# Performance work log

Measured on AMD Instinct MI355X. Metric: run time of the kernel, lower is better.

Reference implementation:

```python
import jax, jax.numpy as jnp
import numpy as np

B, T, C = 2, 2048, 2048
N_HEAD, N_KV_HEAD = 16, 4
HEAD_DIM = C // N_HEAD  # 128
EPS = 1e-6


def rms_norm(x):
    # no learned scale, normalize over head_dim (last axis)
    return x * jax.lax.rsqrt(jnp.mean(jnp.square(x), axis=-1, keepdims=True) + EPS)


def apply_rotary_emb(x, cos, sin):
    # x: [B, T, H, D]; cos/sin: [T, D/2]  (rotate-half RoPE)
    x1, x2 = jnp.split(x, 2, axis=-1)
    c = cos[None, :, None, :]
    s = sin[None, :, None, :]
    return jnp.concatenate([x1 * c - x2 * s, x1 * s + x2 * c], axis=-1)


def setup_inputs() -> dict:
    key = jax.random.key(0)
    ks = jax.random.split(key, 6)
    x = jax.random.normal(ks[0], (B, T, C), dtype=jnp.float32)
    # real rotary tables: theta = 10000^{-2i/D}
    inv_freq = 1.0 / (10000.0 ** (jnp.arange(0, HEAD_DIM, 2, dtype=jnp.float32) / HEAD_DIM))
    angles = jnp.arange(T, dtype=jnp.float32)[:, None] * inv_freq[None, :]  # [T, D/2]
    cos, sin = jnp.cos(angles), jnp.sin(angles)
    std = 0.02
    Wq = jax.random.normal(ks[1], (C, N_HEAD * HEAD_DIM), dtype=jnp.float32) * std
    Wk = jax.random.normal(ks[2], (C, N_KV_HEAD * HEAD_DIM), dtype=jnp.float32) * std
    Wv = jax.random.normal(ks[3], (C, N_KV_HEAD * HEAD_DIM), dtype=jnp.float32) * std
    Wp = jax.random.normal(ks[4], (C, C), dtype=jnp.float32) * std
    return {"x": x, "cos": cos, "sin": sin, "Wq": Wq, "Wk": Wk, "Wv": Wv, "Wp": Wp}


def reference(x, cos, sin, Wq, Wk, Wv, Wp):
    Bx, Tx, Cx = x.shape
    q = (x @ Wq).reshape(Bx, Tx, N_HEAD, HEAD_DIM)
    k = (x @ Wk).reshape(Bx, Tx, N_KV_HEAD, HEAD_DIM)
    v = (x @ Wv).reshape(Bx, Tx, N_KV_HEAD, HEAD_DIM)
    q = rms_norm(apply_rotary_emb(q, cos, sin))
    k = rms_norm(apply_rotary_emb(k, cos, sin))
    # module scales q by 1/sqrt(D) AND nn.dot_product_attention scales again
    q = q * (1.0 / jnp.sqrt(HEAD_DIM))
    # GQA head repeat
    n_rep = N_HEAD // N_KV_HEAD
    k = jnp.repeat(k, n_rep, axis=2)  # [B, T, H, D]
    v = jnp.repeat(v, n_rep, axis=2)
    scores = jnp.einsum("bthd,bshd->bhts", q, k) / jnp.sqrt(jnp.asarray(HEAD_DIM, x.dtype))
    causal = jnp.tril(jnp.ones((Tx, Tx), dtype=bool))  # key <= query
    scores = jnp.where(causal[None, None, :, :], scores, jnp.finfo(scores.dtype).min)
    probs = jax.nn.softmax(scores, axis=-1)
    y = jnp.einsum("bhts,bshd->bthd", probs, v).reshape(Bx, Tx, Cx)
    return y @ Wp
```

## Files before the change

### kernel.cpp

```cpp
#include <hip/hip_runtime.h>
#include <hip/hip_bf16.h>
#include <math.h>

#define B_  2
#define T_  2048
#define C_  2048
#define NH_ 16
#define NKV_ 4
#define HD_ 128
#define NREP_ (NH_/NKV_)

#define QKVLD 3072
#define KOFF  2048
#define VOFF  2560

#define QSCALE 0.01127105500694502f

typedef __bf16 bf16x8 __attribute__((ext_vector_type(8)));
typedef float  f32x4  __attribute__((ext_vector_type(4)));

__device__ inline void gload_lds16(const void* g, void* l) {
    __builtin_amdgcn_global_load_lds((const __attribute__((address_space(1))) void*)g,
                                     (__attribute__((address_space(3))) void*)l, 16, 0, 0);
}

__global__ __launch_bounds__(256) void cast_bf16(const float* __restrict__ src,
                                                 __bf16* __restrict__ dst)
{
    size_t i = ((size_t)blockIdx.x * 256 + threadIdx.x) * 8;
    float4 a = *(const float4*)&src[i];
    float4 b = *(const float4*)&src[i + 4];
    union { __bf16 h[8]; uint4 u; } pk;
    pk.h[0] = (__bf16)a.x; pk.h[1] = (__bf16)a.y; pk.h[2] = (__bf16)a.z; pk.h[3] = (__bf16)a.w;
    pk.h[4] = (__bf16)b.x; pk.h[5] = (__bf16)b.y; pk.h[6] = (__bf16)b.z; pk.h[7] = (__bf16)b.w;
    *(uint4*)&dst[i] = pk.u;
}

__global__ __launch_bounds__(256) void wtrans_qkv(const float* __restrict__ Wq,
                                                  const float* __restrict__ Wk,
                                                  const float* __restrict__ Wv,
                                                  __bf16* __restrict__ dst)
{
    __shared__ float tl[32][33];
    int ct = blockIdx.x;
    int k0 = blockIdx.y * 32;
    const float* src;
    int ncols, c0, dr0;
    if (ct < 64)      { src = Wq; ncols = 2048; c0 = ct * 32;        dr0 = ct * 32; }
    else if (ct < 80) { src = Wk; ncols = 512;  c0 = (ct - 64) * 32; dr0 = KOFF + (ct - 64) * 32; }
    else              { src = Wv; ncols = 512;  c0 = (ct - 80) * 32; dr0 = VOFF + (ct - 80) * 32; }

    int tid = threadIdx.x;
    int r  = tid >> 3;
    int c4 = (tid & 7) * 4;
    float4 v = *(const float4*)&src[(size_t)(k0 + r) * ncols + c0 + c4];
    tl[r][c4] = v.x; tl[r][c4 + 1] = v.y; tl[r][c4 + 2] = v.z; tl[r][c4 + 3] = v.w;
    __syncthreads();
    union { __bf16 h[4]; uint2 u; } pk;
#pragma unroll
    for (int j = 0; j < 4; ++j) pk.h[j] = (__bf16)tl[c4 + j][r];
    *(uint2*)&dst[(size_t)(dr0 + r) * 2048 + k0 + c4] = pk.u;
}

__global__ __launch_bounds__(256) void wtrans(const float* __restrict__ src,
                                              __bf16* __restrict__ dst, int ncols)
{
    __shared__ float tl[32][33];
    int n0 = blockIdx.x * 32;
    int k0 = blockIdx.y * 32;
    int tid = threadIdx.x;
    int r  = tid >> 3;
    int c4 = (tid & 7) * 4;
    float4 v = *(const float4*)&src[(size_t)(k0 + r) * ncols + n0 + c4];
    tl[r][c4] = v.x; tl[r][c4 + 1] = v.y; tl[r][c4 + 2] = v.z; tl[r][c4 + 3] = v.w;
    __syncthreads();
    union { __bf16 h[4]; uint2 u; } pk;
#pragma unroll
    for (int j = 0; j < 4; ++j) pk.h[j] = (__bf16)tl[c4 + j][r];
    *(uint2*)&dst[(size_t)(n0 + r) * 2048 + k0 + c4] = pk.u;
}

template<typename TOUT>
__global__ __launch_bounds__(256) void gemm_bt(const __bf16* __restrict__ A,
                                               const __bf16* __restrict__ Bt,
                                               TOUT* __restrict__ C,
                                               int M, int N, int K, int ldc)
{
    __shared__ __bf16 As[2][128 * 32];
    __shared__ __bf16 Bs[2][128 * 32];

    const int tid  = threadIdx.x;
    const int wv   = tid >> 6;
    const int lane = tid & 63;
    const int grp  = lane >> 4;
    const int id16 = lane & 15;
    const int wr   = wv >> 1;
    const int wc   = wv & 1;

    const int row0 = blockIdx.y * 128;
    const int col0 = blockIdx.x * 128;

    const int sm = tid >> 2;
    const int sk = (tid & 3) << 3;

    const __bf16* ga0 = A  + (size_t)(row0 + sm) * K + sk;
    const __bf16* ga1 = A  + (size_t)(row0 + 64 + sm) * K + sk;
    const __bf16* gb0 = Bt + (size_t)(col0 + sm) * K + sk;
    const __bf16* gb1 = Bt + (size_t)(col0 + 64 + sm) * K + sk;

    f32x4 acc[4][4];
    const f32x4 fz = {0.f, 0.f, 0.f, 0.f};
#pragma unroll
    for (int i = 0; i < 4; ++i)
#pragma unroll
        for (int j = 0; j < 4; ++j) acc[i][j] = fz;

    const int nk = K >> 5;

    {
        __bf16* a0 = &As[0][wv << 9];
        __bf16* b0 = &Bs[0][wv << 9];
        gload_lds16(ga0, a0);
        gload_lds16(ga1, a0 + 2048);
        gload_lds16(gb0, b0);
        gload_lds16(gb1, b0 + 2048);
    }

    for (int kt = 0; kt < nk; ++kt) {
        const int bufc = kt & 1;
        asm volatile("s_waitcnt vmcnt(0)" ::: "memory");
        __syncthreads();

        if (kt + 1 < nk) {
            const int kb = (kt + 1) << 5;
            __bf16* a0 = &As[1 - bufc][wv << 9];
            __bf16* b0 = &Bs[1 - bufc][wv << 9];
            gload_lds16(ga0 + kb, a0);
            gload_lds16(ga1 + kb, a0 + 2048);
            gload_lds16(gb0 + kb, b0);
            gload_lds16(gb1 + kb, b0 + 2048);
        }

        bf16x8 af[4], bfr[4];
#pragma unroll
        for (int i = 0; i < 4; ++i)
            af[i] = *(const bf16x8*)&As[bufc][((wr << 6) + (i << 4) + id16) * 32 + (grp << 3)];
#pragma unroll
        for (int j = 0; j < 4; ++j)
            bfr[j] = *(const bf16x8*)&Bs[bufc][((wc << 6) + (j << 4) + id16) * 32 + (grp << 3)];
#pragma unroll
        for (int i = 0; i < 4; ++i)
#pragma unroll
            for (int j = 0; j < 4; ++j)
                acc[i][j] = __builtin_amdgcn_mfma_f32_16x16x32_bf16(af[i], bfr[j], acc[i][j], 0, 0, 0);
    }

#pragma unroll
    for (int i = 0; i < 4; ++i) {
        int gr = row0 + (wr << 6) + (i << 4) + (grp << 2);
#pragma unroll
        for (int j = 0; j < 4; ++j) {
            int gc = col0 + (wc << 6) + (j << 4) + id16;
#pragma unroll
            for (int r = 0; r < 4; ++r) {
                if constexpr (sizeof(TOUT) == 4)
                    C[(size_t)(gr + r) * ldc + gc] = acc[i][j][r];
                else
                    C[(size_t)(gr + r) * ldc + gc] = (TOUT)acc[i][j][r];
            }
        }
    }
}

__global__ __launch_bounds__(256) void rope_rms_b(__bf16* __restrict__ base,
                                                  const float* __restrict__ cosb,
                                                  const float* __restrict__ sinb,
                                                  int nheads, float scale)
{
    int wid  = blockIdx.x * 4 + (threadIdx.x >> 6);
    int lane = threadIdx.x & 63;
    int bt = wid / nheads;
    int hd = wid % nheads;
    int t  = bt % T_;

    __bf16* p = base + (size_t)bt * QKVLD + hd * HD_;
    float c = cosb[t * 64 + lane];
    float s = sinb[t * 64 + lane];
    float x1 = (float)p[lane];
    float x2 = (float)p[lane + 64];
    float r1 = x1 * c - x2 * s;
    float r2 = x1 * s + x2 * c;
    float ss = r1 * r1 + r2 * r2;
#pragma unroll
    for (int off = 32; off; off >>= 1) ss += __shfl_xor(ss, off, 64);
    float inv = rsqrtf(ss * (1.f / 128.f) + 1e-6f) * scale;
    p[lane]      = (__bf16)(r1 * inv);
    p[lane + 64] = (__bf16)(r2 * inv);
}

__global__ __launch_bounds__(256) void vtrans(const __bf16* __restrict__ qkv,
                                              __bf16* __restrict__ vt)
{
    __shared__ __bf16 tl[32][HD_ + 8];
    int bx  = blockIdx.x;
    int st  = bx & 63;
    int bkv = bx >> 6;
    int b = bkv >> 2, kv = bkv & 3;
    int s0 = st << 5;
    int tid = threadIdx.x;
    {
        int s = tid >> 3;
        int d = (tid & 7) << 4;
        const __bf16* src = qkv + (size_t)(b * T_ + s0 + s) * QKVLD + VOFF + kv * HD_ + d;
        *(bf16x8*)&tl[s][d]     = *(const bf16x8*)src;
        *(bf16x8*)&tl[s][d + 8] = *(const bf16x8*)(src + 8);
    }
    __syncthreads();
    {
        int d  = tid >> 1;
        int sh = (tid & 1) << 4;
        __bf16 tmp[16];
#pragma unroll
        for (int j = 0; j < 16; ++j) tmp[j] = tl[sh + j][d];
        __bf16* dst = vt + ((size_t)(b * NKV_ + kv) * HD_ + d) * T_ + s0 + sh;
        *(bf16x8*)dst       = *(bf16x8*)&tmp[0];
        *(bf16x8*)(dst + 8) = *(bf16x8*)&tmp[8];
    }
}

#define KT2 64
#define PP  72

__global__ __launch_bounds__(256) void attn_mfma2(const __bf16* __restrict__ qkv,
                                                  const __bf16* __restrict__ vbT,
                                                  __bf16* __restrict__ y)
{
    __shared__ __bf16 Ks[2][KT2 * 128];
    __shared__ __bf16 VTs[2][128 * KT2];
    __shared__ __bf16 Ps[4][16 * PP];

    const int tid  = threadIdx.x;
    const int wv   = tid >> 6;
    const int lane = tid & 63;
    const int grp  = lane >> 4;
    const int id16 = lane & 15;

    const int bx = blockIdx.x;
    const int j  = bx & 15;
    const int bh = bx >> 4;
    const int b  = bh >> 4;
    const int h  = bh & 15;
    const int kv = h >> 2;

    const int q0a = j << 6;
    const int q0b = (31 - j) << 6;
    const int NTa = j + 1;
    const int NT  = 33;

    const int l4 = lane >> 4, l8 = lane >> 3;
    size_t koff[4], voff[4];
#pragma unroll
    for (int i = 0; i < 4; ++i) {
        int key = wv * 16 + i * 4 + l4;
        int ch  = (lane & 15) ^ (i * 4 + l4);
        koff[i] = (size_t)key * (QKVLD * 2) + ch * 16;
        int d   = wv * 32 + i * 8 + l8;
        int ch2 = (lane & 7) ^ l8;
        voff[i] = (size_t)d * (T_ * 2) + ch2 * 16;
    }
    const char* kg = (const char*)(qkv + (size_t)b * T_ * QKVLD + KOFF + kv * HD_);
    const char* vg = (const char*)(vbT + ((size_t)(b * NKV_ + kv) * HD_) * T_);

    bf16x8 qf[4], qf2[4];
    {
        const __bf16* qp = qkv + (size_t)(b * T_ + q0a + wv * 16 + id16) * QKVLD + h * HD_ + (grp << 3);
#pragma unroll
        for (int c = 0; c < 4; ++c) qf[c] = *(const bf16x8*)(qp + c * 32);
        const __bf16* qp2 = qkv + (size_t)(b * T_ + q0b + wv * 16 + id16) * QKVLD + h * HD_ + (grp << 3);
#pragma unroll
        for (int c = 0; c < 4; ++c) qf2[c] = *(const bf16x8*)(qp2 + c * 32);
    }

    const f32x4 fz = {0.f, 0.f, 0.f, 0.f};
    f32x4 o[8];
#pragma unroll
    for (int c = 0; c < 8; ++c) o[c] = fz;
    float l_r[4];
#pragma unroll
    for (int r = 0; r < 4; ++r) l_r[r] = 0.f;

    int qbase = q0a + wv * 16;
    int q0c   = q0a;

    {
        __bf16* kl = &Ks[0][(wv * 16) * 128];
        __bf16* vl = &VTs[0][(wv * 32) * 64];
#pragma unroll
        for (int i = 0; i < 4; ++i) gload_lds16(kg + koff[i], kl + i * 4 * 128);
#pragma unroll
        for (int i = 0; i < 4; ++i) gload_lds16(vg + voff[i], vl + i * 8 * 64);
    }

    for (int tt = 0; tt < NT; ++tt) {
        const int bufc = tt & 1;
        asm volatile("s_waitcnt vmcnt(0)" ::: "memory");
        __syncthreads();

        if (tt + 1 < NT) {
            int tn = tt + 1;
            int sn = (tn >= NTa ? tn - NTa : tn) << 6;
            __bf16* kl = &Ks[tn & 1][(wv * 16) * 128];
            __bf16* vl = &VTs[tn & 1][(wv * 32) * 64];
            const char* kp = kg + (size_t)sn * (QKVLD * 2);
            const char* vp = vg + (size_t)sn * 2;
#pragma unroll
            for (int i = 0; i < 4; ++i) gload_lds16(kp + koff[i], kl + i * 4 * 128);
#pragma unroll
            for (int i = 0; i < 4; ++i) gload_lds16(vp + voff[i], vl + i * 8 * 64);
        }

        if (tt == NTa) {
            float inv[4];
#pragma unroll
            for (int r = 0; r < 4; ++r) {
                float l = l_r[r];
                l += __shfl_xor(l, 1, 64);
                l += __shfl_xor(l, 2, 64);
                l += __shfl_xor(l, 4, 64);
                l += __shfl_xor(l, 8, 64);
                inv[r] = 1.f / l;
            }
#pragma unroll
            for (int r = 0; r < 4; ++r) {
                int q = qbase + (grp << 2) + r;
                __bf16* yp = y + (size_t)(b * T_ + q) * C_ + h * HD_ + id16;
#pragma unroll
                for (int c = 0; c < 8; ++c) yp[c * 16] = (__bf16)(o[c][r] * inv[r]);
            }
#pragma unroll
            for (int c = 0; c < 8; ++c) o[c] = fz;
#pragma unroll
            for (int r = 0; r < 4; ++r) l_r[r] = 0.f;
#pragma unroll
            for (int c = 0; c < 4; ++c) qf[c] = qf2[c];
            qbase = q0b + wv * 16;
            q0c   = q0b;
        }

        const int s0 = (tt >= NTa ? tt - NTa : tt) << 6;

        f32x4 S[4];
#pragma unroll
        for (int t = 0; t < 4; ++t) S[t] = fz;
#pragma unroll
        for (int c = 0; c < 4; ++c) {
#pragma unroll
            for (int t = 0; t < 4; ++t) {
                bf16x8 kf = *(const bf16x8*)&Ks[bufc][(t * 16 + id16) * 128 + ((((c << 2) + grp) ^ id16) << 3)];
                S[t] = __builtin_amdgcn_mfma_f32_16x16x32_bf16(qf[c], kf, S[t], 0, 0, 0);
            }
        }
        if (s0 == q0c) {
#pragma unroll
            for (int t = 0; t < 4; ++t)
#pragma unroll
                for (int r = 0; r < 4; ++r)
                    if (s0 + t * 16 + id16 > qbase + (grp << 2) + r) S[t][r] = -1e30f;
        }

#pragma unroll
        for (int t = 0; t < 4; ++t)
#pragma unroll
            for (int r = 0; r < 4; ++r) S[t][r] = exp2f(S[t][r]);
#pragma unroll
        for (int r = 0; r < 4; ++r)
            l_r[r] += (S[0][r] + S[1][r]) + (S[2][r] + S[3][r]);

        __bf16* pw = Ps[wv];
#pragma unroll
        for (int t = 0; t < 4; ++t)
#pragma unroll
            for (int r = 0; r < 4; ++r)
                pw[((grp << 2) + r) * PP + t * 16 + id16] = (__bf16)S[t][r];

        asm volatile("s_waitcnt lgkmcnt(0)" ::: "memory");
        bf16x8 pf0 = *(const bf16x8*)&pw[id16 * PP + (grp << 3)];
        bf16x8 pf1 = *(const bf16x8*)&pw[id16 * PP + 32 + (grp << 3)];

#pragma unroll
        for (int c2 = 0; c2 < 8; ++c2) {
            bf16x8 vf0 = *(const bf16x8*)&VTs[bufc][(c2 * 16 + id16) * 64 + ((grp ^ (id16 & 7)) << 3)];
            o[c2] = __builtin_amdgcn_mfma_f32_16x16x32_bf16(pf0, vf0, o[c2], 0, 0, 0);
            bf16x8 vf1 = *(const bf16x8*)&VTs[bufc][(c2 * 16 + id16) * 64 + (((4 + grp) ^ (id16 & 7)) << 3)];
            o[c2] = __builtin_amdgcn_mfma_f32_16x16x32_bf16(pf1, vf1, o[c2], 0, 0, 0);
        }
    }

    {
        float inv[4];
#pragma unroll
        for (int r = 0; r < 4; ++r) {
            float l = l_r[r];
            l += __shfl_xor(l, 1, 64);
            l += __shfl_xor(l, 2, 64);
            l += __shfl_xor(l, 4, 64);
            l += __shfl_xor(l, 8, 64);
            inv[r] = 1.f / l;
        }
#pragma unroll
        for (int r = 0; r < 4; ++r) {
            int q = qbase + (grp << 2) + r;
            __bf16* yp = y + (size_t)(b * T_ + q) * C_ + h * HD_ + id16;
#pragma unroll
            for (int c = 0; c < 8; ++c) yp[c * 16] = (__bf16)(o[c][r] * inv[r]);
        }
    }
}

extern "C" void kernel_launch(void* const* d_in, const int* in_sizes, int n_in,
                              void* d_out, int out_size, void* d_ws, size_t ws_size,
                              hipStream_t stream)
{
    const float* x    = (const float*)d_in[0];
    const float* cosb = (const float*)d_in[1];
    const float* sinb = (const float*)d_in[2];
    const float* Wq   = (const float*)d_in[3];
    const float* Wk   = (const float*)d_in[4];
    const float* Wv   = (const float*)d_in[5];
    const float* Wp   = (const float*)d_in[6];
    float* out = (float*)d_out;

    const int M = B_ * T_;

    char* w = (char*)d_ws;
    __bf16* xb    = (__bf16*)w;  w += (size_t)M * C_ * 2;
    __bf16* qkv   = (__bf16*)w;  w += (size_t)M * QKVLD * 2;
    __bf16* wqkvT = (__bf16*)w;  w += (size_t)QKVLD * C_ * 2;
    __bf16* wpT   = (__bf16*)w;  w += (size_t)C_ * C_ * 2;
    __bf16* vt    = (__bf16*)w;  w += (size_t)M * NKV_ * HD_ * 2;
    __bf16* y     = (__bf16*)w;

    cast_bf16<<<(M * C_) / 2048, 256, 0, stream>>>(x, xb);
    wtrans_qkv<<<dim3(96, C_ / 32), 256, 0, stream>>>(Wq, Wk, Wv, wqkvT);
    wtrans<<<dim3(C_ / 32, C_ / 32), 256, 0, stream>>>(Wp, wpT, C_);

    gemm_bt<__bf16><<<dim3(QKVLD / 128, M / 128), 256, 0, stream>>>(xb, wqkvT, qkv, M, QKVLD, C_, QKVLD);

    rope_rms_b<<<(M * NH_) / 4, 256, 0, stream>>>(qkv, cosb, sinb, NH_, QSCALE);
    rope_rms_b<<<(M * NKV_) / 4, 256, 0, stream>>>(qkv + KOFF, cosb, sinb, NKV_, 1.0f);

    vtrans<<<B_ * NKV_ * (T_ / 32), 256, 0, stream>>>(qkv, vt);

    attn_mfma2<<<B_ * NH_ * 16, 256, 0, stream>>>(qkv, vt, y);

    gemm_bt<float><<<dim3(C_ / 128, M / 128), 256, 0, stream>>>(y, wpT, out, M, C_, C_, C_);
}
```

Measured before the change: 318.9 us.

## Rewrite attention with 32x32 MFMA, register-resident P, and 128-row query blocks

Replaces the 16x16 MFMA attention kernel with one that uses 32x32x16 MFMA tiles. Each block now handles 128 query rows, with 32 per wave, and blocks are ordered heaviest first in place of the paired light/heavy query scheme. The kernel computes S transposed (K as the A operand) so probabilities can be repacked in registers via a cross-half lane shuffle, removing the LDS round-trip for P. It also adds setprio around the MFMA bursts and a launch bound of two blocks per CU. The cost is more registers, some waves idling on fully masked tiles (they skip with continue), and a different load balance.

```diff
diff --git a/kernel.cpp b/kernel.cpp
--- a/kernel.cpp
+++ b/kernel.cpp
@@ -18,6 +18,7 @@
 
 typedef __bf16 bf16x8 __attribute__((ext_vector_type(8)));
 typedef float  f32x4  __attribute__((ext_vector_type(4)));
+typedef float  f32x16 __attribute__((ext_vector_type(16)));
 
 __device__ inline void gload_lds16(const void* g, void* l) {
     __builtin_amdgcn_global_load_lds((const __attribute__((address_space(1))) void*)g,
@@ -228,77 +229,65 @@
     }
 }
 
-#define KT2 64
-#define PP  72
-
-__global__ __launch_bounds__(256) void attn_mfma2(const __bf16* __restrict__ qkv,
-                                                  const __bf16* __restrict__ vbT,
-                                                  __bf16* __restrict__ y)
-{
-    __shared__ __bf16 Ks[2][KT2 * 128];
-    __shared__ __bf16 VTs[2][128 * KT2];
-    __shared__ __bf16 Ps[4][16 * PP];
+__global__ __launch_bounds__(256, 2) void attn32(const __bf16* __restrict__ qkv,
+                                                 const __bf16* __restrict__ vbT,
+                                                 __bf16* __restrict__ y)
+{
+    __shared__ __bf16 Ks[2][64 * 128];
+    __shared__ __bf16 Vs[2][64 * 128];
 
     const int tid  = threadIdx.x;
     const int wv   = tid >> 6;
     const int lane = tid & 63;
-    const int grp  = lane >> 4;
-    const int id16 = lane & 15;
-
-    const int bx = blockIdx.x;
-    const int j  = bx & 15;
-    const int bh = bx >> 4;
-    const int b  = bh >> 4;
-    const int h  = bh & 15;
-    const int kv = h >> 2;
-
-    const int q0a = j << 6;
-    const int q0b = (31 - j) << 6;
-    const int NTa = j + 1;
-    const int NT  = 33;
-
-    const int l4 = lane >> 4, l8 = lane >> 3;
+    const int l31  = lane & 31;
+    const int h32  = lane >> 5;
+
+    const int bx    = blockIdx.x;
+    const int jslot = bx >> 5;
+    const int bh    = bx & 31;
+    const int b     = bh >> 4;
+    const int h     = bh & 15;
+    const int kv    = h >> 2;
+    const int jj    = (jslot < 8) ? (15 - jslot) : (jslot - 8);
+
+    const int NT  = 2 * jj + 2;
+    const int qw0 = jj * 128 + wv * 32;
+    const int qme = qw0 + l31;
+
     size_t koff[4], voff[4];
 #pragma unroll
     for (int i = 0; i < 4; ++i) {
-        int key = wv * 16 + i * 4 + l4;
-        int ch  = (lane & 15) ^ (i * 4 + l4);
-        koff[i] = (size_t)key * (QKVLD * 2) + ch * 16;
-        int d   = wv * 32 + i * 8 + l8;
-        int ch2 = (lane & 7) ^ l8;
-        voff[i] = (size_t)d * (T_ * 2) + ch2 * 16;
+        int r  = (wv * 4 + i) * 4 + (lane >> 4);
+        int c  = lane & 15;
+        int cs = c ^ (r & 15);
+        koff[i] = (size_t)r * (QKVLD * 2) + (size_t)cs * 16;
+        int d   = r + ((cs >> 3) << 6);
+        voff[i] = (size_t)d * (T_ * 2) + (size_t)(cs & 7) * 16;
     }
     const char* kg = (const char*)(qkv + (size_t)b * T_ * QKVLD + KOFF + kv * HD_);
     const char* vg = (const char*)(vbT + ((size_t)(b * NKV_ + kv) * HD_) * T_);
 
-    bf16x8 qf[4], qf2[4];
+    bf16x8 qf[8];
     {
-        const __bf16* qp = qkv + (size_t)(b * T_ + q0a + wv * 16 + id16) * QKVLD + h * HD_ + (grp << 3);
-#pragma unroll
-        for (int c = 0; c < 4; ++c) qf[c] = *(const bf16x8*)(qp + c * 32);
-        const __bf16* qp2 = qkv + (size_t)(b * T_ + q0b + wv * 16 + id16) * QKVLD + h * HD_ + (grp << 3);
-#pragma unroll
-        for (int c = 0; c < 4; ++c) qf2[c] = *(const bf16x8*)(qp2 + c * 32);
-    }
-
-    const f32x4 fz = {0.f, 0.f, 0.f, 0.f};
-    f32x4 o[8];
-#pragma unroll
-    for (int c = 0; c < 8; ++c) o[c] = fz;
-    float l_r[4];
-#pragma unroll
-    for (int r = 0; r < 4; ++r) l_r[r] = 0.f;
-
-    int qbase = q0a + wv * 16;
-    int q0c   = q0a;
+        const __bf16* qp = qkv + (size_t)(b * T_ + qw0 + l31) * QKVLD + h * HD_ + h32 * 8;
+#pragma unroll
+        for (int s = 0; s < 8; ++s) qf[s] = *(const bf16x8*)(qp + s * 16);
+    }
+
+    f32x16 o[4];
+#pragma unroll
+    for (int dt = 0; dt < 4; ++dt)
+#pragma unroll
+        for (int r = 0; r < 16; ++r) o[dt][r] = 0.f;
+    float l_p = 0.f;
 
     {
-        __bf16* kl = &Ks[0][(wv * 16) * 128];
-        __bf16* vl = &VTs[0][(wv * 32) * 64];
-#pragma unroll
-        for (int i = 0; i < 4; ++i) gload_lds16(kg + koff[i], kl + i * 4 * 128);
-#pragma unroll
-        for (int i = 0; i < 4; ++i) gload_lds16(vg + voff[i], vl + i * 8 * 64);
+        __bf16* kl = &Ks[0][(wv * 4) * 512];
+        __bf16* vl = &Vs[0][(wv * 4) * 512];
+#pragma unroll
+        for (int i = 0; i < 4; ++i) gload_lds16(kg + koff[i], kl + i * 512);
+#pragma unroll
+        for (int i = 0; i < 4; ++i) gload_lds16(vg + voff[i], vl + i * 512);
     }
 
     for (int tt = 0; tt < NT; ++tt) {
@@ -307,114 +296,115 @@
         __syncthreads();
 
         if (tt + 1 < NT) {
-            int tn = tt + 1;
-            int sn = (tn >= NTa ? tn - NTa : tn) << 6;
-            __bf16* kl = &Ks[tn & 1][(wv * 16) * 128];
-            __bf16* vl = &VTs[tn & 1][(wv * 32) * 64];
-            const char* kp = kg + (size_t)sn * (QKVLD * 2);
-            const char* vp = vg + (size_t)sn * 2;
-#pragma unroll
-            for (int i = 0; i < 4; ++i) gload_lds16(kp + koff[i], kl + i * 4 * 128);
-#pragma unroll
-            for (int i = 0; i < 4; ++i) gload_lds16(vp + voff[i], vl + i * 8 * 64);
-        }
-
-        if (tt == NTa) {
-            float inv[4];
-#pragma unroll
-            for (int r = 0; r < 4; ++r) {
-                float l = l_r[r];
-                l += __shfl_xor(l, 1, 64);
-                l += __shfl_xor(l, 2, 64);
-                l += __shfl_xor(l, 4, 64);
-                l += __shfl_xor(l, 8, 64);
-                inv[r] = 1.f / l;
+            const char* kp = kg + (size_t)(tt + 1) * (64 * QKVLD * 2);
+            const char* vp = vg + (size_t)(tt + 1) * (64 * 2);
+            __bf16* kl = &Ks[1 - bufc][(wv * 4) * 512];
+            __bf16* vl = &Vs[1 - bufc][(wv * 4) * 512];
+#pragma unroll
+            for (int i = 0; i < 4; ++i) gload_lds16(kp + koff[i], kl + i * 512);
+#pragma unroll
+            for (int i = 0; i < 4; ++i) gload_lds16(vp + voff[i], vl + i * 512);
+        }
+
+        const int s0 = tt << 6;
+        if (s0 > qw0 + 31) continue;
+
+        f32x16 S0, S1;
+#pragma unroll
+        for (int r = 0; r < 16; ++r) { S0[r] = 0.f; S1[r] = 0.f; }
+        const __bf16* Kb = Ks[bufc];
+        __builtin_amdgcn_s_setprio(1);
+#pragma unroll
+        for (int s = 0; s < 8; ++s) {
+            int ch = s * 2 + h32;
+            bf16x8 kf0 = *(const bf16x8*)&Kb[l31 * 128 + ((ch ^ (l31 & 15)) << 3)];
+            bf16x8 kf1 = *(const bf16x8*)&Kb[(32 + l31) * 128 + ((ch ^ (l31 & 15)) << 3)];
+            S0 = __builtin_amdgcn_mfma_f32_32x32x16_bf16(kf0, qf[s], S0, 0, 0, 0);
+            S1 = __builtin_amdgcn_mfma_f32_32x32x16_bf16(kf1, qf[s], S1, 0, 0, 0);
+        }
+        __builtin_amdgcn_s_setprio(0);
+
+        const bool domask = (s0 + 63 > qw0);
+        uint w[16];
+#pragma unroll
+        for (int i = 0; i < 8; ++i) {
+            const int r0 = 2 * i;
+            float e0 = exp2f(S0[r0]);
+            float e1 = exp2f(S0[r0 + 1]);
+            if (domask) {
+                int k0 = s0 + (r0 & 3) + 8 * (r0 >> 2) + 4 * h32;
+                if (k0     > qme) e0 = 0.f;
+                if (k0 + 1 > qme) e1 = 0.f;
             }
-#pragma unroll
-            for (int r = 0; r < 4; ++r) {
-                int q = qbase + (grp << 2) + r;
-                __bf16* yp = y + (size_t)(b * T_ + q) * C_ + h * HD_ + id16;
-#pragma unroll
-                for (int c = 0; c < 8; ++c) yp[c * 16] = (__bf16)(o[c][r] * inv[r]);
+            l_p += e0 + e1;
+            union { __bf16 h2[2]; uint u; } pk;
+            pk.h2[0] = (__bf16)e0; pk.h2[1] = (__bf16)e1;
+            w[i] = pk.u;
+        }
+#pragma unroll
+        for (int i = 0; i < 8; ++i) {
+            const int r0 = 2 * i;
+            float e0 = exp2f(S1[r0]);
+            float e1 = exp2f(S1[r0 + 1]);
+            if (domask) {
+                int k0 = s0 + 32 + (r0 & 3) + 8 * (r0 >> 2) + 4 * h32;
+                if (k0     > qme) e0 = 0.f;
+                if (k0 + 1 > qme) e1 = 0.f;
             }
-#pragma unroll
-            for (int c = 0; c < 8; ++c) o[c] = fz;
-#pragma unroll
-            for (int r = 0; r < 4; ++r) l_r[r] = 0.f;
-#pragma unroll
-            for (int c = 0; c < 4; ++c) qf[c] = qf2[c];
-            qbase = q0b + wv * 16;
-            q0c   = q0b;
-        }
-
-        const int s0 = (tt >= NTa ? tt - NTa : tt) << 6;
-
-        f32x4 S[4];
-#pragma unroll
-        for (int t = 0; t < 4; ++t) S[t] = fz;
-#pragma unroll
-        for (int c = 0; c < 4; ++c) {
-#pragma unroll
-            for (int t = 0; t < 4; ++t) {
-                bf16x8 kf = *(const bf16x8*)&Ks[bufc][(t * 16 + id16) * 128 + ((((c << 2) + grp) ^ id16) << 3)];
-                S[t] = __builtin_amdgcn_mfma_f32_16x16x32_bf16(qf[c], kf, S[t], 0, 0, 0);
+            l_p += e0 + e1;
+            union { __bf16 h2[2]; uint u; } pk;
+            pk.h2[0] = (__bf16)e0; pk.h2[1] = (__bf16)e1;
+            w[8 + i] = pk.u;
+        }
+
+        uint sw[16];
+#pragma unroll
+        for (int i = 0; i < 16; ++i) sw[i] = (uint)__shfl_xor((int)w[i], 32, 64);
+
+        union U8 { uint u[4]; bf16x8 v; };
+        bf16x8 pf[4];
+#pragma unroll
+        for (int ks = 0; ks < 4; ++ks) {
+            const int bsel = ((ks >> 1) << 3) + ((ks & 1) << 2);
+            U8 t;
+            if (h32 == 0) {
+                t.u[0] = w[bsel];      t.u[1] = w[bsel + 1];
+                t.u[2] = sw[bsel];     t.u[3] = sw[bsel + 1];
+            } else {
+                t.u[0] = sw[bsel + 2]; t.u[1] = sw[bsel + 3];
+                t.u[2] = w[bsel + 2];  t.u[3] = w[bsel + 3];
             }
-        }
-        if (s0 == q0c) {
-#pragma unroll
-            for (int t = 0; t < 4; ++t)
-#pragma unroll
-                for (int r = 0; r < 4; ++r)
-                    if (s0 + t * 16 + id16 > qbase + (grp << 2) + r) S[t][r] = -1e30f;
-        }
-
-#pragma unroll
-        for (int t = 0; t < 4; ++t)
-#pragma unroll
-            for (int r = 0; r < 4; ++r) S[t][r] = exp2f(S[t][r]);
-#pragma unroll
-        for (int r = 0; r < 4; ++r)
-            l_r[r] += (S[0][r] + S[1][r]) + (S[2][r] + S[3][r]);
-
-        __bf16* pw = Ps[wv];
-#pragma unroll
-        for (int t = 0; t < 4; ++t)
-#pragma unroll
-            for (int r = 0; r < 4; ++r)
-                pw[((grp << 2) + r) * PP + t * 16 + id16] = (__bf16)S[t][r];
-
-        asm volatile("s_waitcnt lgkmcnt(0)" ::: "memory");
-        bf16x8 pf0 = *(const bf16x8*)&pw[id16 * PP + (grp << 3)];
-        bf16x8 pf1 = *(const bf16x8*)&pw[id16 * PP + 32 + (grp << 3)];
-
-#pragma unroll
-        for (int c2 = 0; c2 < 8; ++c2) {
-            bf16x8 vf0 = *(const bf16x8*)&VTs[bufc][(c2 * 16 + id16) * 64 + ((grp ^ (id16 & 7)) << 3)];
-            o[c2] = __builtin_amdgcn_mfma_f32_16x16x32_bf16(pf0, vf0, o[c2], 0, 0, 0);
-            bf16x8 vf1 = *(const bf16x8*)&VTs[bufc][(c2 * 16 + id16) * 64 + (((4 + grp) ^ (id16 & 7)) << 3)];
-            o[c2] = __builtin_amdgcn_mfma_f32_16x16x32_bf16(pf1, vf1, o[c2], 0, 0, 0);
-        }
-    }
-
-    {
-        float inv[4];
-#pragma unroll
-        for (int r = 0; r < 4; ++r) {
-            float l = l_r[r];
-            l += __shfl_xor(l, 1, 64);
-            l += __shfl_xor(l, 2, 64);
-            l += __shfl_xor(l, 4, 64);
-            l += __shfl_xor(l, 8, 64);
-            inv[r] = 1.f / l;
-        }
-#pragma unroll
-        for (int r = 0; r < 4; ++r) {
-            int q = qbase + (grp << 2) + r;
-            __bf16* yp = y + (size_t)(b * T_ + q) * C_ + h * HD_ + id16;
-#pragma unroll
-            for (int c = 0; c < 8; ++c) yp[c * 16] = (__bf16)(o[c][r] * inv[r]);
-        }
-    }
+            pf[ks] = t.v;
+        }
+
+        const __bf16* Vb = Vs[bufc];
+        __builtin_amdgcn_s_setprio(1);
+#pragma unroll
+        for (int dt = 0; dt < 4; ++dt) {
+            const int vrow = ((dt & 1) << 5) + l31;
+            const int cb   = (dt >> 1) << 3;
+#pragma unroll
+            for (int ks = 0; ks < 4; ++ks) {
+                int ch = cb + ks * 2 + h32;
+                bf16x8 vf = *(const bf16x8*)&Vb[vrow * 128 + ((ch ^ (vrow & 15)) << 3)];
+                o[dt] = __builtin_amdgcn_mfma_f32_32x32x16_bf16(vf, pf[ks], o[dt], 0, 0, 0);
+            }
+        }
+        __builtin_amdgcn_s_setprio(0);
+    }
+
+    float l  = l_p + __shfl_xor(l_p, 32, 64);
+    float inv = 1.f / l;
+    __bf16* yp = y + (size_t)(b * T_ + qw0 + l31) * C_ + h * HD_;
+#pragma unroll
+    for (int dt = 0; dt < 4; ++dt)
+#pragma unroll
+        for (int g = 0; g < 4; ++g) {
+            union { __bf16 h4[4]; uint2 u; } pk;
+#pragma unroll
+            for (int e = 0; e < 4; ++e) pk.h4[e] = (__bf16)(o[dt][4 * g + e] * inv);
+            *(uint2*)&yp[dt * 32 + 8 * g + 4 * h32] = pk.u;
+        }
 }
 
 extern "C" void kernel_launch(void* const* d_in, const int* in_sizes, int n_in,
@@ -451,7 +441,7 @@
 
     vtrans<<<B_ * NKV_ * (T_ / 32), 256, 0, stream>>>(qkv, vt);
 
-    attn_mfma2<<<B_ * NH_ * 16, 256, 0, stream>>>(qkv, vt, y);
+    attn32<<<512, 256, 0, stream>>>(qkv, vt, y);
 
     gemm_bt<float><<<dim3(C_ / 128, M / 128), 256, 0, stream>>>(y, wpT, out, M, C_, C_, C_);
 }
```

Measured after the change: 332.7 us. 4.3% more time.
